# Kernel tuning notes

Hardware: AMD Instinct MI355X
Metric: run time of the kernel (lower is better)

Reference implementation:

```python
import jax, jax.numpy as jnp
import numpy as np

L = 8192            # sequence length
V = 100000          # vocab size
E = 256             # embedding dim
H = 512             # lstm hidden dim (bidirectional total)
HD = H // 2         # per-direction hidden
TAGS = 32
T = TAGS + 2        # tagset + START/STOP
START = T - 2       # START_TAG = -2
STOP = T - 1        # STOP_TAG = -1
NEG = -10000.0


def setup_inputs() -> dict:
    key = jax.random.key(0)
    ks = jax.random.split(key, 11)
    s = 0.05
    return {
        "input_words": jax.random.randint(ks[0], (L,), 0, V),
        "embed": jax.random.normal(ks[1], (V, E), dtype=jnp.float32) * s,
        "Wih_f": jax.random.normal(ks[2], (4 * HD, E), dtype=jnp.float32) * s,
        "Whh_f": jax.random.normal(ks[3], (4 * HD, HD), dtype=jnp.float32) * s,
        "b_f": jax.random.normal(ks[4], (4 * HD,), dtype=jnp.float32) * s,
        "Wih_b": jax.random.normal(ks[5], (4 * HD, E), dtype=jnp.float32) * s,
        "Whh_b": jax.random.normal(ks[6], (4 * HD, HD), dtype=jnp.float32) * s,
        "b_b": jax.random.normal(ks[7], (4 * HD,), dtype=jnp.float32) * s,
        "W_out": jax.random.normal(ks[8], (T, H), dtype=jnp.float32) * s,
        "b_out": jax.random.normal(ks[9], (T,), dtype=jnp.float32) * s,
        "transitions": jax.random.normal(ks[10], (T, T), dtype=jnp.float32),
    }


def _lstm_dir(x, Wih, Whh, b, reverse):
    # single-layer LSTM, one direction; torch gate order i, f, g, o
    def step(carry, xt):
        h, c = carry
        g = xt @ Wih.T + h @ Whh.T + b
        i, f, gg, o = jnp.split(g, 4)
        i = jax.nn.sigmoid(i)
        f = jax.nn.sigmoid(f)
        gg = jnp.tanh(gg)
        o = jax.nn.sigmoid(o)
        c = f * c + i * gg
        h = o * jnp.tanh(c)
        return (h, c), h

    init = (jnp.zeros((HD,), x.dtype), jnp.zeros((HD,), x.dtype))
    _, hs = jax.lax.scan(step, init, x, reverse=reverse)
    return hs  # (L, HD)


def _crf_marginals(feats, transitions):
    lse = jax.nn.logsumexp
    # forward algorithm: alpha_t[j] = lse_i(alpha_{t-1}[i] + trans[j,i]) + feat_t[j]
    def fstep(alpha, feat):
        new = lse(alpha[None, :] + transitions, axis=1) + feat
        return new, new

    alpha0 = jnp.full((T,), NEG, feats.dtype).at[START].set(0.0)
    alphaL, log_alpha = jax.lax.scan(fstep, alpha0, feats)  # (L, T)

    # backward algorithm, replicating repo's init: beta_L[j] = lse_i(trans[i, j])
    beta_last = lse(transitions, axis=0)

    # beta_t[j] = lse_i(beta_{t+1}[i] + feat_{t+1}[i] + trans[i, j])
    def bstep(beta, feat_next):
        new = lse((beta + feat_next)[:, None] + transitions, axis=0)
        return new, new

    _, betas = jax.lax.scan(bstep, beta_last, feats[1:], reverse=True)
    log_beta = jnp.concatenate([betas, beta_last[None]], axis=0)  # (L, T)
    return log_alpha + log_beta


def reference(input_words, embed, Wih_f, Whh_f, b_f, Wih_b, Whh_b, b_b,
              W_out, b_out, transitions):
    x = embed[input_words]                           # (L, E)
    hf = _lstm_dir(x, Wih_f, Whh_f, b_f, reverse=False)
    hb = _lstm_dir(x, Wih_b, Whh_b, b_b, reverse=True)
    lstm_out = jnp.concatenate([hf, hb], axis=-1)    # (L, H)
    feats = lstm_out @ W_out.T + b_out               # (L, T)
    score = _crf_marginals(feats, transitions)       # (L, T)
    tags = jnp.argmax(score, axis=1)                 # (L,)
    return score, tags
```

## Files before the change

kernel.cpp:

```cpp
#include <hip/hip_runtime.h>
#include <cstdint>
#include <cstddef>

#define LSEQ 8192
#define NT   34
#define NP   36
#define SCH  64
#define CCH  128
#define F_L2E 1.4426950408889634f
#define F_LN2 0.6931471805599453f

#if __has_builtin(__builtin_amdgcn_sdot4)
#define DOT4(a,b,c) __builtin_amdgcn_sdot4((a),(b),(c),false)
#else
__device__ __forceinline__ int dot4_fb(int a,int b,int c){
  c += (int)(signed char)(a & 0xff)        * (int)(signed char)(b & 0xff);
  c += (int)(signed char)((a>>8) & 0xff)   * (int)(signed char)((b>>8) & 0xff);
  c += (int)(signed char)((a>>16) & 0xff)  * (int)(signed char)((b>>16) & 0xff);
  c += (a>>24) * (b>>24);
  return c;
}
#define DOT4(a,b,c) dot4_fb((a),(b),(c))
#endif

#if __has_builtin(__builtin_amdgcn_global_load_lds)
#define HAS_GLL 1
#else
#define HAS_GLL 0
#endif

__device__ __forceinline__ float ex2(float x){
#if __has_builtin(__builtin_amdgcn_exp2f)
  return __builtin_amdgcn_exp2f(x);
#else
  return exp2f(x);
#endif
}
__device__ __forceinline__ float lg2(float x){
#if __has_builtin(__builtin_amdgcn_logf)
  return __builtin_amdgcn_logf(x);
#else
  return __log2f(x);
#endif
}

__device__ __forceinline__ float sigf(float x){
  return __fdividef(1.f, 1.f + ex2(-F_L2E * x));
}
__device__ __forceinline__ float tanhf_fast(float x){
  return 1.f - __fdividef(2.f, ex2(2.f * F_L2E * x) + 1.f);
}

__device__ __forceinline__ int qreduce(int x){
#if __has_builtin(__builtin_amdgcn_mov_dpp)
  x += __builtin_amdgcn_mov_dpp(x, 0xB1, 0xF, 0xF, true);
  x += __builtin_amdgcn_mov_dpp(x, 0x4E, 0xF, 0xF, true);
#else
  x += __shfl_xor(x, 1);
  x += __shfl_xor(x, 2);
#endif
  return x;
}

__device__ __forceinline__ void barrier_lds(){
  asm volatile("s_waitcnt lgkmcnt(0)\n\ts_barrier" ::: "memory");
}

__global__ void k_quant(const float* __restrict__ Whh_f,
                        const float* __restrict__ Whh_b,
                        int* __restrict__ Wq, float* __restrict__ fac){
  int bid = blockIdx.x;
  int dir = bid >> 10;
  int r   = bid & 1023;
  int i   = threadIdx.x;
  const float* W = (dir ? Whh_b : Whh_f) + r * 256 + i * 4;
  float w0 = W[0], w1 = W[1], w2 = W[2], w3 = W[3];
  float m = fmaxf(fmaxf(fabsf(w0), fabsf(w1)), fmaxf(fabsf(w2), fabsf(w3)));
  for (int s = 32; s; s >>= 1) m = fmaxf(m, __shfl_xor(m, s));
  float scale = (m > 0.f) ? m / 127.f : 1.f;
  float inv = __fdividef(1.f, scale);
  int q0 = (int)rintf(w0 * inv), q1 = (int)rintf(w1 * inv);
  int q2 = (int)rintf(w2 * inv), q3 = (int)rintf(w3 * inv);
  q0 = max(-127, min(127, q0)); q1 = max(-127, min(127, q1));
  q2 = max(-127, min(127, q2)); q3 = max(-127, min(127, q3));
  int p = (q0 & 255) | ((q1 & 255) << 8) | ((q2 & 255) << 16) | ((q3 & 255) << 24);
  Wq[(dir << 16) + (r << 6) + i] = p;
  if (i == 0) fac[(dir << 10) + r] = scale * (1.f / 127.f);
}

__global__ void k_gproj(const int* __restrict__ words,
                        const float* __restrict__ embed,
                        const float* __restrict__ Wih_f, const float* __restrict__ b_f,
                        const float* __restrict__ Wih_b, const float* __restrict__ b_b,
                        float* __restrict__ G_f, float* __restrict__ G_b){
  int dir = blockIdx.y;
  const float* Wih = dir ? Wih_b : Wih_f;
  const float* bb  = dir ? b_b  : b_f;
  float* G = dir ? G_b : G_f;
  int t0 = blockIdx.x * 16;
  __shared__ __align__(16) float X[16 * 256];
  for (int idx = threadIdx.x; idx < 16 * 256; idx += 256) {
    int tt = idx >> 8, e = idx & 255;
    X[idx] = embed[(size_t)words[t0 + tt] * 256 + e];
  }
  __syncthreads();
  const float4* X4 = (const float4*)X;
  for (int rb = 0; rb < 4; rb++) {
    int r = rb * 256 + threadIdx.x;
    float bv = bb[r];
    float acc[16];
#pragma unroll
    for (int tt = 0; tt < 16; tt++) acc[tt] = bv;
    const float4* W4 = (const float4*)(Wih + (size_t)r * 256);
    for (int eb = 0; eb < 64; eb++) {
      float4 w = W4[eb];
#pragma unroll
      for (int tt = 0; tt < 16; tt++) {
        float4 x = X4[tt * 64 + eb];
        acc[tt] += w.x * x.x + w.y * x.y + w.z * x.z + w.w * x.w;
      }
    }
    for (int tt = 0; tt < 16; tt++)
      G[(size_t)(t0 + tt) * 1024 + (threadIdx.x << 2) + rb] = acc[tt];
  }
}

__global__ __launch_bounds__(512, 2) void k_lstm(const int* __restrict__ Wq,
                                                 const float* __restrict__ fac,
                                                 const float* __restrict__ G_f,
                                                 const float* __restrict__ G_b,
                                                 float* __restrict__ hf,
                                                 float* __restrict__ hb){
  int dir = blockIdx.x;
  const int* Wqd = Wq + (dir << 16);
  const float* facp = fac + (dir << 10);
  const float* G = dir ? G_b : G_f;
  float* hout = dir ? hb : hf;
  int tid = threadIdx.x;
  int ln  = tid & 63;
  int wv  = tid >> 6;
  int q   = tid >> 2;
  int kq  = tid & 3;
  int u   = (q << 1) + (tid & 1);

  __shared__ __align__(16) float GL[2][4 * 1024];
  __shared__ __align__(16) int h8[2][64];

  int4 w4[8][4];
#pragma unroll
  for (int g = 0; g < 4; g++) {
#pragma unroll
    for (int uu = 0; uu < 2; uu++) {
      int r = (q << 1) + uu + (g << 8);
      const int4* p = (const int4*)(Wqd + (r << 6) + (kq << 4));
      w4[g * 2 + uu][0] = p[0]; w4[g * 2 + uu][1] = p[1];
      w4[g * 2 + uu][2] = p[2]; w4[g * 2 + uu][3] = p[3];
    }
  }
  float fI = facp[u], fF = facp[u + 256], fG = facp[u + 512], fO = facp[u + 768];
  if (tid < 64) h8[0][tid] = 0;
  float c = 0.f;

  auto stage = [&](int cn) {
    int half = cn & 1;
    int gt0 = dir ? (8191 - (cn * 4 + 3)) : (cn * 4);
    const char* src = (const char*)(G + (size_t)gt0 * 1024) + (wv << 11) + (ln << 4);
    char* dst = (char*)&GL[half][0] + (wv << 11);
#pragma unroll
    for (int i = 0; i < 2; i++) {
#if HAS_GLL
      __builtin_amdgcn_global_load_lds(
          (const __attribute__((address_space(1))) unsigned int*)(src + (i << 10)),
          (__attribute__((address_space(3))) unsigned int*)(dst + (i << 10)),
          16, 0, 0);
#else
      *(float4*)(dst + (i << 10) + (ln << 4)) = *(const float4*)(src + (i << 10));
#endif
    }
  };

  auto step = [&](int t, const float* Grow, const int* bufR, int* bufW) {
    const int4* hs = (const int4*)((const char*)bufR + (kq << 6));
    int4 h0 = hs[0], h1 = hs[1], h2 = hs[2], h3 = hs[3];
    int acc[8];
#pragma unroll
    for (int m = 0; m < 8; m++) {
      int a = 0;
      a = DOT4(w4[m][0].x, h0.x, a); a = DOT4(w4[m][0].y, h0.y, a);
      a = DOT4(w4[m][0].z, h0.z, a); a = DOT4(w4[m][0].w, h0.w, a);
      a = DOT4(w4[m][1].x, h1.x, a); a = DOT4(w4[m][1].y, h1.y, a);
      a = DOT4(w4[m][1].z, h1.z, a); a = DOT4(w4[m][1].w, h1.w, a);
      a = DOT4(w4[m][2].x, h2.x, a); a = DOT4(w4[m][2].y, h2.y, a);
      a = DOT4(w4[m][2].z, h2.z, a); a = DOT4(w4[m][2].w, h2.w, a);
      a = DOT4(w4[m][3].x, h3.x, a); a = DOT4(w4[m][3].y, h3.y, a);
      a = DOT4(w4[m][3].z, h3.z, a); a = DOT4(w4[m][3].w, h3.w, a);
      acc[m] = a;
    }
#pragma unroll
    for (int m = 0; m < 8; m++) acc[m] = qreduce(acc[m]);
    int p = tid & 1;
    int aI = p ? acc[1] : acc[0];
    int aF = p ? acc[3] : acc[2];
    int aG = p ? acc[5] : acc[4];
    int aO = p ? acc[7] : acc[6];
    float4 gv = ((const float4*)Grow)[u];
    float ri = (float)aI * fI + gv.x;
    float rf = (float)aF * fF + gv.y;
    float rg = (float)aG * fG + gv.z;
    float ro = (float)aO * fO + gv.w;
    float is = sigf(ri), fs = sigf(rf);
    float gt = tanhf_fast(rg), os = sigf(ro);
    c = fs * c + is * gt;
    float h = os * tanhf_fast(c);
    if ((tid & 3) < 2) {
      int time = dir ? (8191 - t) : t;
      hout[(size_t)time * 256 + u] = h;
      ((signed char*)bufW)[u] = (signed char)(int)rintf(h * 127.f);
    }
  };

  stage(0);
  asm volatile("s_waitcnt vmcnt(0)" ::: "memory");
  __syncthreads();

  for (int cn = 0; cn < 2048; ++cn) {
    if (cn + 1 < 2048) stage(cn + 1);
    const float* Hc = GL[cn & 1];
    int tb = cn << 2;
#pragma unroll
    for (int s = 0; s < 4; ++s) {
      int row = dir ? (3 - s) : s;
      const float* Grow = Hc + (row << 10);
      int t = tb + s;
      if ((s & 1) == 0) step(t, Grow, h8[0], h8[1]);
      else              step(t, Grow, h8[1], h8[0]);
      if (s == 3) {
        asm volatile("s_waitcnt vmcnt(0) lgkmcnt(0)\n\ts_barrier" ::: "memory");
      } else {
        barrier_lds();
      }
    }
  }
}

__global__ void k_feats(const float* __restrict__ hf, const float* __restrict__ hb,
                        const float* __restrict__ W_out, const float* __restrict__ b_out,
                        float* __restrict__ feats){
  int t0 = blockIdx.x * 16;
  for (int oi = threadIdx.x; oi < 16 * NT; oi += 256) {
    int tt = oi / NT;
    int tag = oi - tt * NT;
    int t = t0 + tt;
    const float4* w4 = (const float4*)(W_out + (size_t)tag * 512);
    const float4* a4 = (const float4*)(hf + (size_t)t * 256);
    const float4* c4 = (const float4*)(hb + (size_t)t * 256);
    float acc = b_out[tag];
    for (int k = 0; k < 64; k++) {
      float4 w = w4[k]; float4 h = a4[k];
      acc += w.x * h.x + w.y * h.y + w.z * h.z + w.w * h.w;
    }
    for (int k = 0; k < 64; k++) {
      float4 w = w4[64 + k]; float4 h = c4[k];
      acc += w.x * h.x + w.y * h.y + w.z * h.z + w.w * h.w;
    }
    feats[(size_t)t * NT + tag] = acc;
  }
}

__global__ __launch_bounds__(320) void k_crf_p1(const float* __restrict__ feats,
                                                const float* __restrict__ trans,
                                                float* __restrict__ Pg,
                                                float* __restrict__ rmaxG){
  int dir = blockIdx.x >> 7;
  int c   = blockIdx.x & (CCH - 1);
  int tid = threadIdx.x;
  int t0  = c * SCH;

  __shared__ __align__(16) float TRM[NT * NP];
  __shared__ float Fe[(SCH + 1) * NT];
  __shared__ __align__(16) float Pbuf[2][NT * NP];
  __shared__ float CM[NP];
  __shared__ float RMs[NT];

  for (int idx = tid; idx < NT * NT; idx += 320) {
    int j = idx / NT, k = idx - j * NT;
    float v = (dir == 0) ? trans[j * NT + k] : trans[k * NT + j];
    TRM[j * NP + k] = v * F_L2E;
  }
  for (int idx = tid; idx < (SCH + 1) * NT; idx += 320) {
    int s = idx / NT, j = idx - s * NT;
    int t = t0 + s; if (t > LSEQ - 1) t = LSEQ - 1;
    Fe[idx] = feats[(size_t)t * NT + j] * F_L2E;
  }
  for (int idx = tid; idx < NT * NP; idx += 320) {
    int k = idx / NP, i = idx - k * NP;
    Pbuf[0][idx] = (i < NT && i == k) ? 0.f : -1e30f;
  }
  if (tid < NP) CM[tid] = (tid < NT) ? 0.f : -1e30f;
  __syncthreads();
  if (tid < NT) {
    float m = -3e38f;
    for (int k = 0; k < NT; k++) m = fmaxf(m, TRM[tid * NP + k]);
    RMs[tid] = m;
  }
  __syncthreads();
  for (int idx = tid; idx < NT * NT; idx += 320) {
    int j = idx / NT, k = idx - j * NT;
    TRM[j * NP + k] -= RMs[j];
  }
  __syncthreads();

  int cur = 0;
  int j = tid / 9, g = tid - (tid / 9) * 9;
  bool act = (tid < 306);
  int i0 = 4 * g;

  for (int s = 0; s < SCH; s++) {
    int t = (dir == 0) ? (t0 + s) : (t0 + SCH - 1 - s);
    if (dir == 1 && t == LSEQ - 1) continue;
    const float* Pc = Pbuf[cur];
    float* Pn = Pbuf[cur ^ 1];
    if (act) {
      float cm0 = CM[i0], cm1 = CM[i0 + 1], cm2 = CM[i0 + 2], cm3 = CM[i0 + 3];
      float s0 = 0, s1 = 0, s2 = 0, s3 = 0;
      const float* trp = TRM + j * NP;
      const float* fep = Fe + (t + 1 - t0) * NT;
#pragma unroll
      for (int k = 0; k < NT; k++) {
        float trv = trp[k];
        if (dir == 1) trv += fep[k];
        float4 p = *(const float4*)&Pc[k * NP + i0];
        s0 += ex2(trv + p.x - cm0);
        s1 += ex2(trv + p.y - cm1);
        s2 += ex2(trv + p.z - cm2);
        s3 += ex2(trv + p.w - cm3);
      }
      float base = RMs[j] + ((dir == 0) ? Fe[(t - t0) * NT + j] : 0.f);
      float4 o;
      o.x = base + cm0 + lg2(s0);
      o.y = base + cm1 + lg2(s1);
      o.z = (i0 + 2 < NT) ? (base + cm2 + lg2(s2)) : -1e30f;
      o.w = (i0 + 3 < NT) ? (base + cm3 + lg2(s3)) : -1e30f;
      *(float4*)&Pn[j * NP + i0] = o;
    }
    __syncthreads();
    if (tid < NP) {
      float m = -3e38f;
      const float* col = Pn + tid;
      for (int k = 0; k < NT; k++) m = fmaxf(m, col[k * NP]);
      CM[tid] = m;
    }
    cur ^= 1;
    __syncthreads();
  }

  const float* Pf = Pbuf[cur];
  size_t base = (size_t)((dir << 7) + c) * (NT * NP);
  for (int idx = tid; idx < NT * NP; idx += 320)
    Pg[base + idx] = Pf[idx];
  if (tid < NT) {
    float m = -3e38f;
    for (int i = 0; i < NT; i++) m = fmaxf(m, Pf[tid * NP + i]);
    rmaxG[((dir << 7) + c) * NT + tid] = m;
  }
}

__global__ void k_crf_p2(const float* __restrict__ trans,
                         const float* __restrict__ Pg,
                         const float* __restrict__ rmaxG,
                         float* __restrict__ vIn){
  int dir = blockIdx.x;
  int lane = threadIdx.x;
  bool a = (lane < NT);
  int j = a ? lane : 0;
  __shared__ float V[NP];

  float v;
  if (dir == 0) {
    v = (lane == 32) ? 0.f : -10000.f * F_L2E;
  } else {
    float m = -3e38f;
    for (int i = 0; i < NT; i++) m = fmaxf(m, trans[i * NT + j]);
    float s = 0.f;
    for (int i = 0; i < NT; i++) s += ex2((trans[i * NT + j] - m) * F_L2E);
    v = m * F_L2E + lg2(s);
  }
  if (lane < NP) V[lane] = -1e30f;
  barrier_lds();
  if (a) V[j] = v;
  barrier_lds();
  float vm = a ? v : -3e38f;
  for (int off = 32; off; off >>= 1) vm = fmaxf(vm, __shfl_xor(vm, off));

  if (a) {
    int c0 = (dir == 0) ? 0 : (CCH - 1);
    vIn[((size_t)(dir << 7) + c0) * NP + j] = v;
  }

  for (int it = 0; it < CCH - 1; it++) {
    int c = (dir == 0) ? it : (CCH - 1 - it);
    const float* row = Pg + ((size_t)(dir << 7) + c) * (NT * NP) + j * NP;
    float rm = rmaxG[((dir << 7) + c) * NT + j];
    float m = rm + vm;
    float s = 0.f;
#pragma unroll
    for (int k = 0; k < NP; k += 4) {
      float4 p = *(const float4*)&row[k];
      s += ex2(p.x + V[k]     - m);
      s += ex2(p.y + V[k + 1] - m);
      s += ex2(p.z + V[k + 2] - m);
      s += ex2(p.w + V[k + 3] - m);
    }
    float nv = m + lg2(s);
    if (a) V[j] = nv;
    barrier_lds();
    float x = a ? nv : -3e38f;
    for (int off = 32; off; off >>= 1) x = fmaxf(x, __shfl_xor(x, off));
    vm = x;
    int cn = (dir == 0) ? (c + 1) : (c - 1);
    if (a) vIn[((size_t)(dir << 7) + cn) * NP + j] = nv;
  }
}

__global__ void k_crf_p3(const float* __restrict__ feats,
                         const float* __restrict__ trans,
                         const float* __restrict__ vIn,
                         float* __restrict__ wsA,
                         float* __restrict__ wsB){
  int dir = blockIdx.x >> 7;
  int c   = blockIdx.x & (CCH - 1);
  int lane = threadIdx.x;
  int t0 = c * SCH;
  bool a = (lane < NT);
  int j = a ? lane : 0;
  __shared__ float A[NP];
  __shared__ float U[NP];

  float trr[NT];
  float rm = -3e38f;
#pragma unroll
  for (int k = 0; k < NT; k++) {
    float vv = (dir == 0) ? trans[j * NT + k] : trans[k * NT + j];
    trr[k] = vv * F_L2E;
    rm = fmaxf(rm, trr[k]);
  }
  if (lane < NP) { A[lane] = -1e30f; U[lane] = -1e30f; }
  float v0 = vIn[((size_t)(dir << 7) + c) * NP + j];
  barrier_lds();
  if (a) A[j] = v0;
  barrier_lds();
  float am = a ? v0 : -3e38f;
  for (int off = 32; off; off >>= 1) am = fmaxf(am, __shfl_xor(am, off));

  if (dir == 0) {
    float fe = feats[(size_t)t0 * NT + j] * F_L2E;
    for (int s = 0; s < SCH; s++) {
      int t = t0 + s;
      int tn = (t + 1 < LSEQ) ? t + 1 : LSEQ - 1;
      float fe_n = feats[(size_t)tn * NT + j] * F_L2E;
      float m = rm + am;
      float ss = 0.f;
#pragma unroll
      for (int k = 0; k < NT; k++) ss += ex2(trr[k] + A[k] - m);
      float out = m + lg2(ss) + fe;
      if (a) wsA[(size_t)t * NT + j] = out * F_LN2;
      if (a) A[j] = out;
      barrier_lds();
      float x = a ? out : -3e38f;
      for (int off = 32; off; off >>= 1) x = fmaxf(x, __shfl_xor(x, off));
      am = x;
      fe = fe_n;
    }
  } else {
    float b = v0;
    int tfirst = t0 + SCH; if (tfirst > LSEQ - 1) tfirst = LSEQ - 1;
    float fe = feats[(size_t)tfirst * NT + j] * F_L2E;
    for (int s = 0; s < SCH; s++) {
      int t = t0 + SCH - 1 - s;
      float fe_n = feats[(size_t)t * NT + j] * F_L2E;
      float out;
      if (t == LSEQ - 1) {
        out = b;
      } else {
        if (a) U[j] = b + fe;
        barrier_lds();
        float um = a ? U[j] : -3e38f;
        for (int off = 32; off; off >>= 1) um = fmaxf(um, __shfl_xor(um, off));
        float m = rm + um;
        float ss = 0.f;
#pragma unroll
        for (int k = 0; k < NT; k++) ss += ex2(trr[k] + U[k] - m);
        out = m + lg2(ss);
        barrier_lds();
      }
      if (a) wsB[(size_t)t * NT + j] = out * F_LN2;
      b = out;
      fe = fe_n;
    }
  }
}

__global__ void k_finish(const float* __restrict__ wsA, const float* __restrict__ wsB,
                         float* __restrict__ out){
  int t = blockIdx.x * 256 + threadIdx.x;
  float m = -3e38f; int bi = 0;
  for (int i = 0; i < NT; i++) {
    float sc = wsA[(size_t)t * NT + i] + wsB[(size_t)t * NT + i];
    out[(size_t)t * NT + i] = sc;
    if (sc > m) { m = sc; bi = i; }
  }
  out[(size_t)LSEQ * NT + t] = (float)bi;
}

extern "C" void kernel_launch(void* const* d_in, const int* in_sizes, int n_in,
                              void* d_out, int out_size, void* d_ws, size_t ws_size,
                              hipStream_t stream) {
  const int*   words  = (const int*)  d_in[0];
  const float* embed  = (const float*)d_in[1];
  const float* Wih_f  = (const float*)d_in[2];
  const float* Whh_f  = (const float*)d_in[3];
  const float* b_f    = (const float*)d_in[4];
  const float* Wih_b  = (const float*)d_in[5];
  const float* Whh_b  = (const float*)d_in[6];
  const float* b_b    = (const float*)d_in[7];
  const float* W_out  = (const float*)d_in[8];
  const float* b_out  = (const float*)d_in[9];
  const float* trans  = (const float*)d_in[10];
  float* out = (float*)d_out;

  float* wsf = (float*)d_ws;
  size_t off = 0;
  float* G_f   = wsf + off; off += (size_t)LSEQ * 1024;
  float* G_b   = wsf + off; off += (size_t)LSEQ * 1024;
  float* hf    = wsf + off; off += (size_t)LSEQ * 256;
  float* hb    = wsf + off; off += (size_t)LSEQ * 256;
  float* feats = wsf + off; off += (size_t)LSEQ * NT + 16;
  float* wsA   = wsf + off; off += (size_t)LSEQ * NT + 16;
  float* wsB   = wsf + off; off += (size_t)LSEQ * NT + 16;
  float* fac   = wsf + off; off += 2048;
  int*   Wq    = (int*)(wsf + off); off += 2 * 1024 * 64;
  float* Pg    = G_f;
  float* rmaxG = G_f + 256 * (NT * NP);
  float* vIn   = rmaxG + 256 * NT + 32;

  k_quant<<<2048, 64, 0, stream>>>(Whh_f, Whh_b, Wq, fac);
  k_gproj<<<dim3(512, 2), 256, 0, stream>>>(words, embed, Wih_f, b_f, Wih_b, b_b, G_f, G_b);
  k_lstm<<<2, 512, 0, stream>>>(Wq, fac, G_f, G_b, hf, hb);
  k_feats<<<512, 256, 0, stream>>>(hf, hb, W_out, b_out, feats);
  k_crf_p1<<<256, 320, 0, stream>>>(feats, trans, Pg, rmaxG);
  k_crf_p2<<<2, 64, 0, stream>>>(trans, Pg, rmaxG, vIn);
  k_crf_p3<<<256, 64, 0, stream>>>(feats, trans, vIn, wsA, wsB);
  k_finish<<<32, 256, 0, stream>>>(wsA, wsB, out);
}
```

Baseline: 9.454 ms.

## Use int8 MFMA for the recurrent LSTM matvec instead of sdot4

The per-step recurrent h·Whh product moves from per-thread sdot4 chains with DPP quad reductions to v_mfma_i32_16x16x64_i8. Quantized weights stay resident in registers in MFMA operand layout, and the int8 h vector is broadcast as the B operand. Gate pre-activations go through an LDS buffer, and an extra barrier sits before 256 threads run the elementwise cell update. The aim is to cut the ALU instruction count on the serial recurrence path. The cost is MFMA latency chains, 15 of 16 output columns computed and discarded, and a second barrier per time step.

Result: faster. 8.705 ms (-7.9%).

```diff
diff --git a/kernel.cpp b/kernel.cpp
--- a/kernel.cpp
+++ b/kernel.cpp
@@ -10,18 +10,7 @@
 #define F_L2E 1.4426950408889634f
 #define F_LN2 0.6931471805599453f
 
-#if __has_builtin(__builtin_amdgcn_sdot4)
-#define DOT4(a,b,c) __builtin_amdgcn_sdot4((a),(b),(c),false)
-#else
-__device__ __forceinline__ int dot4_fb(int a,int b,int c){
-  c += (int)(signed char)(a & 0xff)        * (int)(signed char)(b & 0xff);
-  c += (int)(signed char)((a>>8) & 0xff)   * (int)(signed char)((b>>8) & 0xff);
-  c += (int)(signed char)((a>>16) & 0xff)  * (int)(signed char)((b>>16) & 0xff);
-  c += (a>>24) * (b>>24);
-  return c;
-}
-#define DOT4(a,b,c) dot4_fb((a),(b),(c))
-#endif
+typedef int v4i __attribute__((ext_vector_type(4)));
 
 #if __has_builtin(__builtin_amdgcn_global_load_lds)
 #define HAS_GLL 1
@@ -51,15 +40,9 @@
   return 1.f - __fdividef(2.f, ex2(2.f * F_L2E * x) + 1.f);
 }
 
-__device__ __forceinline__ int qreduce(int x){
-#if __has_builtin(__builtin_amdgcn_mov_dpp)
-  x += __builtin_amdgcn_mov_dpp(x, 0xB1, 0xF, 0xF, true);
-  x += __builtin_amdgcn_mov_dpp(x, 0x4E, 0xF, 0xF, true);
-#else
-  x += __shfl_xor(x, 1);
-  x += __shfl_xor(x, 2);
-#endif
-  return x;
+__device__ __forceinline__ v4i mfma_i8(v4i a, v4i b, v4i c){
+  asm("v_mfma_i32_16x16x64_i8 %0, %1, %2, %0" : "+v"(c) : "v"(a), "v"(b));
+  return c;
 }
 
 __device__ __forceinline__ void barrier_lds(){
@@ -139,27 +122,32 @@
   int tid = threadIdx.x;
   int ln  = tid & 63;
   int wv  = tid >> 6;
-  int q   = tid >> 2;
-  int kq  = tid & 3;
-  int u   = (q << 1) + (tid & 1);
+  int lg  = ln >> 4;
+  int lr  = ln & 15;
 
   __shared__ __align__(16) float GL[2][4 * 1024];
-  __shared__ __align__(16) int h8[2][64];
-
-  int4 w4[8][4];
-#pragma unroll
-  for (int g = 0; g < 4; g++) {
-#pragma unroll
-    for (int uu = 0; uu < 2; uu++) {
-      int r = (q << 1) + uu + (g << 8);
-      const int4* p = (const int4*)(Wqd + (r << 6) + (kq << 4));
-      w4[g * 2 + uu][0] = p[0]; w4[g * 2 + uu][1] = p[1];
-      w4[g * 2 + uu][2] = p[2]; w4[g * 2 + uu][3] = p[3];
-    }
-  }
-  float fI = facp[u], fF = facp[u + 256], fG = facp[u + 512], fO = facp[u + 768];
-  if (tid < 64) h8[0][tid] = 0;
+  __shared__ __align__(16) int h8c[2][64];
+  __shared__ __align__(16) int graw[1024];
+
+  v4i wgt[4][2][4];
+#pragma unroll
+  for (int g = 0; g < 4; g++)
+#pragma unroll
+    for (int h = 0; h < 2; h++) {
+      int R = g * 256 + wv * 32 + h * 16 + lr;
+#pragma unroll
+      for (int ks = 0; ks < 4; ks++)
+        wgt[g][h][ks] = *(const v4i*)(Wqd + R * 64 + ks * 16 + lg * 4);
+    }
+
+  float fI = 0.f, fF = 0.f, fG = 0.f, fO = 0.f;
+  if (tid < 256) {
+    fI = facp[tid]; fF = facp[tid + 256];
+    fG = facp[tid + 512]; fO = facp[tid + 768];
+  }
+  if (tid < 64) h8c[0][tid] = 0;
   float c = 0.f;
+  v4i zero = {0, 0, 0, 0};
 
   auto stage = [&](int cn) {
     int half = cn & 1;
@@ -179,61 +167,53 @@
     }
   };
 
-  auto step = [&](int t, const float* Grow, const int* bufR, int* bufW) {
-    const int4* hs = (const int4*)((const char*)bufR + (kq << 6));
-    int4 h0 = hs[0], h1 = hs[1], h2 = hs[2], h3 = hs[3];
-    int acc[8];
-#pragma unroll
-    for (int m = 0; m < 8; m++) {
-      int a = 0;
-      a = DOT4(w4[m][0].x, h0.x, a); a = DOT4(w4[m][0].y, h0.y, a);
-      a = DOT4(w4[m][0].z, h0.z, a); a = DOT4(w4[m][0].w, h0.w, a);
-      a = DOT4(w4[m][1].x, h1.x, a); a = DOT4(w4[m][1].y, h1.y, a);
-      a = DOT4(w4[m][1].z, h1.z, a); a = DOT4(w4[m][1].w, h1.w, a);
-      a = DOT4(w4[m][2].x, h2.x, a); a = DOT4(w4[m][2].y, h2.y, a);
-      a = DOT4(w4[m][2].z, h2.z, a); a = DOT4(w4[m][2].w, h2.w, a);
-      a = DOT4(w4[m][3].x, h3.x, a); a = DOT4(w4[m][3].y, h3.y, a);
-      a = DOT4(w4[m][3].z, h3.z, a); a = DOT4(w4[m][3].w, h3.w, a);
-      acc[m] = a;
-    }
-#pragma unroll
-    for (int m = 0; m < 8; m++) acc[m] = qreduce(acc[m]);
-    int p = tid & 1;
-    int aI = p ? acc[1] : acc[0];
-    int aF = p ? acc[3] : acc[2];
-    int aG = p ? acc[5] : acc[4];
-    int aO = p ? acc[7] : acc[6];
-    float4 gv = ((const float4*)Grow)[u];
-    float ri = (float)aI * fI + gv.x;
-    float rf = (float)aF * fF + gv.y;
-    float rg = (float)aG * fG + gv.z;
-    float ro = (float)aO * fO + gv.w;
-    float is = sigf(ri), fs = sigf(rf);
-    float gt = tanhf_fast(rg), os = sigf(ro);
-    c = fs * c + is * gt;
-    float h = os * tanhf_fast(c);
-    if ((tid & 3) < 2) {
-      int time = dir ? (8191 - t) : t;
-      hout[(size_t)time * 256 + u] = h;
-      ((signed char*)bufW)[u] = (signed char)(int)rintf(h * 127.f);
-    }
+  auto stepA = [&](const int* hbuf) {
+    const v4i* hb4 = (const v4i*)hbuf;
+    v4i b0 = hb4[lg], b1 = hb4[4 + lg], b2 = hb4[8 + lg], b3 = hb4[12 + lg];
+#pragma unroll
+    for (int g = 0; g < 4; g++)
+#pragma unroll
+      for (int h = 0; h < 2; h++) {
+        v4i a = mfma_i8(wgt[g][h][0], b0, zero);
+        a = mfma_i8(wgt[g][h][1], b1, a);
+        a = mfma_i8(wgt[g][h][2], b2, a);
+        a = mfma_i8(wgt[g][h][3], b3, a);
+        if (lr == 0)
+          *(v4i*)&graw[g * 256 + wv * 32 + h * 16 + lg * 4] = a;
+      }
   };
 
   stage(0);
   asm volatile("s_waitcnt vmcnt(0)" ::: "memory");
   __syncthreads();
 
+  int cur = 0;
   for (int cn = 0; cn < 2048; ++cn) {
     if (cn + 1 < 2048) stage(cn + 1);
     const float* Hc = GL[cn & 1];
-    int tb = cn << 2;
 #pragma unroll
     for (int s = 0; s < 4; ++s) {
       int row = dir ? (3 - s) : s;
-      const float* Grow = Hc + (row << 10);
-      int t = tb + s;
-      if ((s & 1) == 0) step(t, Grow, h8[0], h8[1]);
-      else              step(t, Grow, h8[1], h8[0]);
+      int t = (cn << 2) + s;
+      stepA(h8c[cur]);
+      barrier_lds();
+      if (tid < 256) {
+        int u = tid;
+        int aI = graw[u], aF = graw[256 + u], aG = graw[512 + u], aO = graw[768 + u];
+        float4 gv = ((const float4*)(Hc + (row << 10)))[u];
+        float ri = (float)aI * fI + gv.x;
+        float rf = (float)aF * fF + gv.y;
+        float rg = (float)aG * fG + gv.z;
+        float ro = (float)aO * fO + gv.w;
+        float is = sigf(ri), fs = sigf(rf);
+        float gt = tanhf_fast(rg), os = sigf(ro);
+        c = fs * c + is * gt;
+        float hv = os * tanhf_fast(c);
+        int time = dir ? (8191 - t) : t;
+        hout[(size_t)time * 256 + u] = hv;
+        ((signed char*)h8c[cur ^ 1])[u] = (signed char)(int)rintf(hv * 127.f);
+      }
+      cur ^= 1;
       if (s == 3) {
         asm volatile("s_waitcnt vmcnt(0) lgkmcnt(0)\n\ts_barrier" ::: "memory");
       } else {
```
